# Kernel optimization log

Hardware: AMD Instinct MI355X
Metric: run time of the kernel (lower is better)

Reference implementation:

```python
import jax, jax.numpy as jnp
import numpy as np

C = 96          # channels (= output_dim)
NUM_HEADS = 6
DILS = (1, 2, 3)
KS_ATT = 3      # dilate-attention kernel size
KS_COR = 5      # self-correlation kernel size
PAD_COR = 2
LN_EPS = 1e-5


def _unfold(x, k, dil, pad):
    # torch.nn.Unfold(kernel=k, dilation=dil, padding=pad, stride=1)
    # x: [B, C, H, W] -> [B, C, k*k, H, W] (channel-major, kernel row-major)
    B, c, H, W = x.shape
    xp = jnp.pad(x, ((0, 0), (0, 0), (pad, pad), (pad, pad)))
    patches = [xp[:, :, i * dil:i * dil + H, j * dil:j * dil + W]
               for i in range(k) for j in range(k)]
    return jnp.stack(patches, axis=2)


def _layernorm(x, g, b):
    m = jnp.mean(x, axis=-1, keepdims=True)
    v = jnp.mean((x - m) ** 2, axis=-1, keepdims=True)
    return (x - m) * jax.lax.rsqrt(v + LN_EPS) * g + b


def _dilate_attn(q, k, v, dil, head_dim, scale):
    # q,k,v: [B, cb, H, W] with cb = C // num_dilation
    B, cb, H, W = q.shape
    heads = cb // head_dim
    qf = q.reshape(B, heads, head_dim, H * W)                                  # bhdn
    kp = _unfold(k, KS_ATT, dil, dil).reshape(B, heads, head_dim, KS_ATT * KS_ATT, H * W)
    attn = jax.nn.softmax(jnp.einsum('bhdn,bhdkn->bhnk', qf, kp) * scale, axis=-1)
    vp = _unfold(v, KS_ATT, dil, dil).reshape(B, heads, head_dim, KS_ATT * KS_ATT, H * W)
    out = jnp.einsum('bhnk,bhdkn->bnhd', attn, vp)                             # [B,HW,heads,hd]
    return out.reshape(B, H, W, cb)


def _forward(x, g1, b1, Wqkv, bqkv, Wproj, bproj, g2, b2, W1, bm1, W2, bm2):
    B, Cc, H, W = x.shape
    nd = len(DILS)
    head_dim = Cc // NUM_HEADS
    scale = head_dim ** (-0.5)

    xh = jnp.transpose(x, (0, 2, 3, 1))                                        # [B,H,W,C]

    # --- MultiDilatelocalAttention block ---
    y = _layernorm(xh, g1, b1)
    qkv = jnp.einsum('bhwc,oc->bhwo', y, Wqkv) + bqkv                          # 1x1 conv == linear
    qkv = jnp.transpose(qkv, (0, 3, 1, 2)).reshape(B, 3, nd, Cc // nd, H, W)
    outs = []
    for i, d in enumerate(DILS):
        outs.append(_dilate_attn(qkv[:, 0, i], qkv[:, 1, i], qkv[:, 2, i], d, head_dim, scale))
    a = jnp.concatenate(outs, axis=-1)                                         # dilation-major channels
    a = a @ Wproj.T + bproj
    xh = xh + a

    # --- MLP block ---
    z = _layernorm(xh, g2, b2)
    z = jax.nn.gelu(z @ W1.T + bm1, approximate=False) @ W2.T + bm2
    xh = xh + z

    # --- self-correlation ---
    xc = jnp.transpose(xh, (0, 3, 1, 2))                                       # [B,C,H,W]
    xc = jax.nn.relu(xc)
    nrm = jnp.sqrt(jnp.sum(xc * xc, axis=1, keepdims=True))
    xc = xc / jnp.maximum(nrm, 1e-12)                                          # F.normalize dim=1
    pat = _unfold(xc, KS_COR, 1, PAD_COR)                                      # [B,C,25,H,W]
    out = pat.reshape(B, Cc, KS_COR, KS_COR, H, W) * xc[:, :, None, None]
    return jnp.transpose(out, (0, 1, 4, 5, 2, 3))                              # [B,C,H,W,5,5]


def setup_inputs() -> dict:
    key = jax.random.key(0)
    ks = jax.random.split(key, 8)
    B, H, W = 8, 64, 64
    s = 0.02
    return {
        'x': jax.random.normal(ks[0], (B, C, H, W), jnp.float32),
        'g1': jnp.ones((C,), jnp.float32),
        'b1': jnp.zeros((C,), jnp.float32),
        'Wqkv': jax.random.normal(ks[1], (3 * C, C), jnp.float32) * s,
        'bqkv': jnp.zeros((3 * C,), jnp.float32),
        'Wproj': jax.random.normal(ks[2], (C, C), jnp.float32) * s,
        'bproj': jnp.zeros((C,), jnp.float32),
        'g2': jnp.ones((C,), jnp.float32),
        'b2': jnp.zeros((C,), jnp.float32),
        'W1': jax.random.normal(ks[3], (4 * C, C), jnp.float32) * s,
        'bm1': jnp.zeros((4 * C,), jnp.float32),
        'W2': jax.random.normal(ks[4], (C, 4 * C), jnp.float32) * s,
        'bm2': jnp.zeros((C,), jnp.float32),
    }


def reference(x, g1, b1, Wqkv, bqkv, Wproj, bproj, g2, b2, W1, bm1, W2, bm2):
    return _forward(x, g1, b1, Wqkv, bqkv, Wproj, bproj, g2, b2, W1, bm1, W2, bm2)
```

## Files before the change

### kernel.cpp

```cpp
#include <hip/hip_runtime.h>
#include <math.h>

#define NN 4096
#define BN 32768
#define CSTR 66

using short8 = __attribute__((ext_vector_type(8))) short;
using f32x4  = __attribute__((ext_vector_type(4))) float;
typedef unsigned short ushort_t;

__device__ inline unsigned f2bfu(float f) {
    unsigned u = __builtin_bit_cast(unsigned, f);
    u += 0x7FFFu + ((u >> 16) & 1u);
    return u >> 16;
}
__device__ inline ushort_t f2bf(float f) { return (ushort_t)f2bfu(f); }
__device__ inline unsigned pack2(float a, float b) { return f2bfu(a) | (f2bfu(b) << 16); }
__device__ inline float bflo(unsigned u) { return __builtin_bit_cast(float, u << 16); }
__device__ inline float bfhi(unsigned u) { return __builtin_bit_cast(float, u & 0xFFFF0000u); }

__device__ inline float gelu_f(float v) {
    float xx = v * 0.70710678118654752f;
    float a  = fabsf(xx);
    float t  = 1.0f / (1.0f + 0.3275911f * a);
    float p  = t*(0.254829592f + t*(-0.284496736f + t*(1.421413741f + t*(-1.453152027f + t*1.061405429f))));
    float erfv = 1.0f - p * __expf(-xx*xx);
    erfv = copysignf(erfv, xx);
    return 0.5f * v * (1.0f + erfv);
}

__device__ inline void stage_w(const unsigned* __restrict__ wbf, int stage,
                               ushort_t* dst, int wv, int lane) {
    const unsigned* src = wbf + (long)stage * 5120 + lane * 4;
    #pragma unroll
    for (int i = 0; i < 5; ++i) {
        int chunk = wv + 4 * i;
        __builtin_amdgcn_global_load_lds(
            (const __attribute__((address_space(1))) unsigned*)(src + chunk * 256),
            (__attribute__((address_space(3))) unsigned*)(dst + chunk * 512),
            16, 0, 0);
    }
}

#define MFMA_GEMM6(ACC, APTR, BPTR)                                              \
    _Pragma("unroll")                                                            \
    for (int kc = 0; kc < 3; ++kc) {                                             \
        short8 a_ = *(const short8*)&(APTR)[(wv*16 + ln)*104 + kc*32 + qd*8];    \
        _Pragma("unroll")                                                        \
        for (int t = 0; t < 6; ++t) {                                            \
            short8 b_ = *(const short8*)&(BPTR)[(t*16 + ln)*104 + kc*32 + qd*8]; \
            ACC[t] = __builtin_amdgcn_mfma_f32_16x16x32_bf16(a_, b_, ACC[t], 0, 0, 0); \
        }                                                                        \
    }

#define MFMA_GEMM6R(ACC, AF, BPTR)                                               \
    _Pragma("unroll")                                                            \
    for (int kc = 0; kc < 3; ++kc) {                                             \
        _Pragma("unroll")                                                        \
        for (int t = 0; t < 6; ++t) {                                            \
            short8 b_ = *(const short8*)&(BPTR)[(t*16 + ln)*104 + kc*32 + qd*8]; \
            ACC[t] = __builtin_amdgcn_mfma_f32_16x16x32_bf16(AF[kc], b_, ACC[t], 0, 0, 0); \
        }                                                                        \
    }

#define LN_FRAGS(AF, CS, G, B)                                                   \
    {                                                                            \
        const int p_ = wv*16 + ln;                                               \
        float xv_[24]; float s_ = 0.f, ss_ = 0.f;                                \
        _Pragma("unroll")                                                        \
        for (int kc = 0; kc < 3; ++kc)                                           \
            _Pragma("unroll")                                                    \
            for (int j = 0; j < 8; ++j) {                                        \
                float v_ = (CS)[(kc*32 + qd*8 + j)*CSTR + p_];                   \
                xv_[kc*8+j] = v_; s_ += v_; ss_ += v_*v_;                        \
            }                                                                    \
        s_  += __shfl_xor(s_, 16);  s_  += __shfl_xor(s_, 32);                   \
        ss_ += __shfl_xor(ss_, 16); ss_ += __shfl_xor(ss_, 32);                  \
        float m_ = s_ * (1.f/96.f);                                              \
        float rs_ = rsqrtf(ss_ * (1.f/96.f) - m_*m_ + 1e-5f);                    \
        _Pragma("unroll")                                                        \
        for (int kc = 0; kc < 3; ++kc)                                           \
            _Pragma("unroll")                                                    \
            for (int h = 0; h < 2; ++h) {                                        \
                int c0_ = kc*32 + qd*8 + h*4;                                    \
                float4 g4_ = *(const float4*)&(G)[c0_];                          \
                float4 b4_ = *(const float4*)&(B)[c0_];                          \
                (AF)[kc][h*4+0] = (short)f2bf((xv_[kc*8+h*4+0]-m_)*rs_*g4_.x + b4_.x); \
                (AF)[kc][h*4+1] = (short)f2bf((xv_[kc*8+h*4+1]-m_)*rs_*g4_.y + b4_.y); \
                (AF)[kc][h*4+2] = (short)f2bf((xv_[kc*8+h*4+2]-m_)*rs_*g4_.z + b4_.z); \
                (AF)[kc][h*4+3] = (short)f2bf((xv_[kc*8+h*4+3]-m_)*rs_*g4_.w + b4_.w); \
            }                                                                    \
    }

__global__ __launch_bounds__(256) void k0_pack(
    const float* __restrict__ Wqkv, const float* __restrict__ Wproj,
    const float* __restrict__ W1, const float* __restrict__ W2,
    unsigned* __restrict__ wbf)
{
    int d = blockIdx.x * 256 + threadIdx.x;
    int s = d / 5120, r = d - s * 5120;
    int o = r / 52, qp = r - o * 52;
    unsigned val = 0u;
    if (o < 96 && qp < 48) {
        int q = qp * 2;
        float2 w2;
        if (s == 0)      w2 = *(const float2*)&Wqkv[(long)o * 96 + q];
        else if (s == 1) w2 = *(const float2*)&Wqkv[(long)(96 + o) * 96 + q];
        else if (s == 2) w2 = *(const float2*)&Wqkv[(long)(192 + o) * 96 + q];
        else if (s == 3) w2 = *(const float2*)&Wproj[(long)o * 96 + q];
        else if (((s - 4) & 1) == 0) { int kb = (s - 4) >> 1; w2 = *(const float2*)&W1[(long)(kb * 96 + o) * 96 + q]; }
        else                         { int kb = (s - 4) >> 1; w2 = *(const float2*)&W2[(long)o * 384 + kb * 96 + q]; }
        val = pack2(w2.x, w2.y);
    }
    wbf[d] = val;
}

__global__ __launch_bounds__(256, 2) void k1_ln_kv(
    const float* __restrict__ x, const float* __restrict__ g1, const float* __restrict__ b1,
    const float* __restrict__ bqkv, const unsigned* __restrict__ wbf,
    unsigned* __restrict__ kvt32)
{
    __shared__ __align__(16) float    Cs[96 * CSTR];
    __shared__ __align__(16) ushort_t Bs[2][10240];
    const int tid = threadIdx.x;
    const int bid = blockIdx.x;
    const int wg  = ((bid & 7) << 6) | (bid >> 3);
    const long bn0 = (long)wg << 6;
    const int b  = (int)(bn0 >> 12);
    const int n0 = (int)(bn0 & 4095);
    const int lane = tid & 63, wv = tid >> 6;
    const int ln = lane & 15, qd = lane >> 4;

    stage_w(wbf, 1, &Bs[0][0], wv, lane);
    stage_w(wbf, 2, &Bs[1][0], wv, lane);
    for (int i = 0; i < 6; ++i) {
        int idx = i * 256 + tid;
        int c = idx >> 4, p4 = idx & 15;
        float4 v = *(const float4*)&x[((long)(b * 96 + c) << 12) + n0 + p4 * 4];
        float* dst = &Cs[c * CSTR + p4 * 4];
        dst[0] = v.x; dst[1] = v.y; dst[2] = v.z; dst[3] = v.w;
    }
    __syncthreads();
    short8 af[3];
    LN_FRAGS(af, Cs, g1, b1);
    f32x4 acck[6];
    #pragma unroll
    for (int t = 0; t < 6; ++t) acck[t] = (f32x4){0.f,0.f,0.f,0.f};
    MFMA_GEMM6R(acck, af, Bs[0]);
    __syncthreads();
    #pragma unroll
    for (int t = 0; t < 6; ++t)
        #pragma unroll
        for (int r = 0; r < 4; ++r)
            Cs[(t*16 + ln)*CSTR + (wv*16 + qd*4 + r)] = acck[t][r];
    __syncthreads();
    f32x4 accv[6];
    #pragma unroll
    for (int t = 0; t < 6; ++t) accv[t] = (f32x4){0.f,0.f,0.f,0.f};
    for (int i = 0; i < 12; ++i) {
        int idx = i * 256 + tid;
        int cp = idx / 64, p = idx % 64;
        int c = 2 * cp;
        kvt32[((long)(b*96 + cp) << 12) + n0 + p] =
            pack2(Cs[c*CSTR + p] + bqkv[96 + c], Cs[(c+1)*CSTR + p] + bqkv[96 + c + 1]);
    }
    MFMA_GEMM6R(accv, af, Bs[1]);
    __syncthreads();
    #pragma unroll
    for (int t = 0; t < 6; ++t)
        #pragma unroll
        for (int r = 0; r < 4; ++r)
            Cs[(t*16 + ln)*CSTR + (wv*16 + qd*4 + r)] = accv[t][r];
    __syncthreads();
    for (int i = 0; i < 12; ++i) {
        int idx = i * 256 + tid;
        int cp = idx / 64, p = idx % 64;
        int c = 2 * cp;
        kvt32[((long)(b*96 + 48 + cp) << 12) + n0 + p] =
            pack2(Cs[c*CSTR + p] + bqkv[192 + c], Cs[(c+1)*CSTR + p] + bqkv[192 + c + 1]);
    }
}

__global__ __launch_bounds__(256, 2) void k2345(
    const unsigned* __restrict__ kvt32, const float* __restrict__ x,
    const float* __restrict__ g1, const float* __restrict__ b1,
    const float* __restrict__ bqkv, const unsigned* __restrict__ wbf,
    const float* __restrict__ bproj,
    const float* __restrict__ g2, const float* __restrict__ b2,
    const float* __restrict__ bm1, const float* __restrict__ bm2,
    float* __restrict__ xcn)
{
    __shared__ __align__(16) float    Cs[96 * CSTR];
    __shared__ __align__(16) ushort_t As[64 * 104];
    __shared__ __align__(16) ushort_t Bs[2][10240];
    __shared__ float lnr[64];
    ushort_t* Hs = (ushort_t*)Cs;
    const int tid = threadIdx.x;
    const int bid = blockIdx.x;
    const int wg  = ((bid & 7) << 6) | (bid >> 3);
    const long bn0 = (long)wg << 6;
    const int b  = (int)(bn0 >> 12);
    const int n0 = (int)(bn0 & 4095);
    const int h0 = n0 >> 6;
    const int lane = tid & 63, wv = tid >> 6;
    const int ln = lane & 15, qd = lane >> 4;

    stage_w(wbf, 0, &Bs[0][0], wv, lane);
    stage_w(wbf, 3, &Bs[1][0], wv, lane);
    for (int i = 0; i < 6; ++i) {
        int idx = i * 256 + tid;
        int c = idx >> 4, p4 = idx & 15;
        float4 v = *(const float4*)&x[((long)(b * 96 + c) << 12) + n0 + p4 * 4];
        float* dst = &Cs[c * CSTR + p4 * 4];
        dst[0] = v.x; dst[1] = v.y; dst[2] = v.z; dst[3] = v.w;
    }
    __syncthreads();
    {
        short8 af[3];
        LN_FRAGS(af, Cs, g1, b1);
        f32x4 acc[6];
        #pragma unroll
        for (int t = 0; t < 6; ++t) acc[t] = (f32x4){0.f,0.f,0.f,0.f};
        MFMA_GEMM6R(acc, af, Bs[0]);
        #pragma unroll
        for (int t = 0; t < 6; ++t) {
            float bias = bqkv[t*16 + ln];
            #pragma unroll
            for (int r = 0; r < 4; ++r)
                As[(wv*16 + qd*4 + r)*104 + t*16 + ln] = f2bf(acc[t][r] + bias);
        }
    }
    __syncthreads();
    stage_w(wbf, 4, &Bs[0][0], wv, lane);
    for (int it = 0; it < 2; ++it) {
        int item = it * 256 + tid;
        if (item < 384) {
            int p = item & 63;
            int r = item >> 6;
            int head = r & 1, di = r >> 1;
            int dil = di + 1;
            int cp0 = di*16 + head*8;
            const unsigned* K = kvt32 + ((long)(b*96 +      cp0) << 12);
            const unsigned* V = kvt32 + ((long)(b*96 + 48 + cp0) << 12);
            int w = p;

            float q[16];
            #pragma unroll
            for (int j = 0; j < 8; ++j) {
                unsigned u = *(const unsigned*)&As[p * 104 + 2*(cp0 + j)];
                q[2*j] = bflo(u); q[2*j+1] = bfhi(u);
            }
            float logits[9];
            #pragma unroll
            for (int ki = 0; ki < 3; ++ki)
                #pragma unroll
                for (int kj = 0; kj < 3; ++kj) {
                    int hh = h0 + (ki-1)*dil, ww = w + (kj-1)*dil;
                    float l = 0.f;
                    if ((unsigned)hh < 64u && (unsigned)ww < 64u) {
                        int nn = (hh << 6) + ww;
                        #pragma unroll
                        for (int j = 0; j < 8; ++j) {
                            unsigned u = K[((long)j << 12) + nn];
                            l += q[2*j] * bflo(u) + q[2*j+1] * bfhi(u);
                        }
                    }
                    logits[ki*3 + kj] = l * 0.25f;
                }
            float m = logits[0];
            #pragma unroll
            for (int k = 1; k < 9; ++k) m = fmaxf(m, logits[k]);
            float e[9], s = 0.f;
            #pragma unroll
            for (int k = 0; k < 9; ++k) { e[k] = __expf(logits[k] - m); s += e[k]; }
            float inv = 1.f / s;
            float o[16];
            #pragma unroll
            for (int d = 0; d < 16; ++d) o[d] = 0.f;
            #pragma unroll
            for (int ki = 0; ki < 3; ++ki)
                #pragma unroll
                for (int kj = 0; kj < 3; ++kj) {
                    int hh = h0 + (ki-1)*dil, ww = w + (kj-1)*dil;
                    if ((unsigned)hh < 64u && (unsigned)ww < 64u) {
                        int nn = (hh << 6) + ww;
                        float wgt = e[ki*3 + kj] * inv;
                        #pragma unroll
                        for (int j = 0; j < 8; ++j) {
                            unsigned u = V[((long)j << 12) + nn];
                            o[2*j]   += wgt * bflo(u);
                            o[2*j+1] += wgt * bfhi(u);
                        }
                    }
                }
            #pragma unroll
            for (int j = 0; j < 8; ++j)
                *(unsigned*)&As[p * 104 + 2*(cp0 + j)] = pack2(o[2*j], o[2*j+1]);
        }
    }
    __syncthreads();
    float resid[24];
    {
        f32x4 acc[6];
        #pragma unroll
        for (int t = 0; t < 6; ++t) acc[t] = (f32x4){0.f,0.f,0.f,0.f};
        MFMA_GEMM6(acc, As, Bs[1]);
        #pragma unroll
        for (int t = 0; t < 6; ++t) {
            int oc = t*16 + ln;
            float bias = bproj[oc];
            #pragma unroll
            for (int r = 0; r < 4; ++r) {
                int p = wv*16 + qd*4 + r;
                float v = acc[t][r] + bias + Cs[oc*CSTR + p];
                resid[t*4 + r] = v;
                Cs[oc*CSTR + p] = v;
            }
        }
    }
    __syncthreads();
    stage_w(wbf, 5, &Bs[1][0], wv, lane);
    short8 zf[3];
    LN_FRAGS(zf, Cs, g2, b2);
    __syncthreads();
    f32x4 acc2[6];
    #pragma unroll
    for (int t = 0; t < 6; ++t) acc2[t] = (f32x4){0.f,0.f,0.f,0.f};
    for (int kb = 0; kb < 4; ++kb) {
        f32x4 acch[6];
        #pragma unroll
        for (int t = 0; t < 6; ++t) acch[t] = (f32x4){0.f,0.f,0.f,0.f};
        MFMA_GEMM6R(acch, zf, Bs[0]);
        #pragma unroll
        for (int t = 0; t < 6; ++t) {
            float bias = bm1[kb*96 + t*16 + ln];
            #pragma unroll
            for (int r = 0; r < 4; ++r)
                Hs[(wv*16 + qd*4 + r)*104 + t*16 + ln] = f2bf(gelu_f(acch[t][r] + bias));
        }
        __syncthreads();
        if (kb < 3) stage_w(wbf, 6 + 2*kb, &Bs[0][0], wv, lane);
        MFMA_GEMM6(acc2, Hs, Bs[1]);
        __syncthreads();
        if (kb < 3) stage_w(wbf, 7 + 2*kb, &Bs[1][0], wv, lane);
    }
    #pragma unroll
    for (int t = 0; t < 6; ++t) {
        int oc = t*16 + ln;
        float bias = bm2[oc];
        #pragma unroll
        for (int r = 0; r < 4; ++r) {
            int p = wv*16 + qd*4 + r;
            float v = acc2[t][r] + bias + resid[t*4 + r];
            Cs[oc*CSTR + p] = fmaxf(v, 0.f);
        }
    }
    __syncthreads();
    {
        int p = tid >> 2, part = tid & 3, c0 = part * 24;
        float ss = 0.f;
        for (int c = c0; c < c0 + 24; ++c) { float v = Cs[c*CSTR + p]; ss += v*v; }
        ss += __shfl_xor(ss, 1); ss += __shfl_xor(ss, 2);
        if (part == 0) lnr[p] = 1.f / fmaxf(sqrtf(ss), 1e-12f);
    }
    __syncthreads();
    for (int i = 0; i < 12; ++i) {
        int idx = i * 256 + tid;
        int p = idx / 48, cp = idx % 48;
        float inv = lnr[p];
        float2 v = make_float2(Cs[(2*cp)*CSTR + p] * inv, Cs[(2*cp+1)*CSTR + p] * inv);
        *(float2*)&xcn[(bn0 + p) * 96 + 2*cp] = v;
    }
}

__global__ __launch_bounds__(256) void k6_selfcorr(
    const float* __restrict__ xcn, float* __restrict__ out)
{
    __shared__ float xt[5 * 20 * 97];
    const int tid = threadIdx.x;
    const int wc = blockIdx.x;
    const int h  = blockIdx.y;
    const int b  = blockIdx.z;
    const int w0 = wc * 16;

    const f32x4* xcn4 = (const f32x4*)xcn;
    for (int i = 0; i < 10; ++i) {
        int idx = i * 256 + tid;
        if (idx < 2400) {
            int r = idx / 480;
            int rem = idx - r * 480;
            int wi = rem / 24, c4 = rem - wi * 24;
            int hh = h + r - 2, ww = w0 + wi - 2;
            f32x4 v = (f32x4){0.f, 0.f, 0.f, 0.f};
            if ((unsigned)hh < 64u && (unsigned)ww < 64u)
                v = xcn4[(((long)b << 12) + (hh << 6) + ww) * 24 + c4];
            float* dst = &xt[(r * 20 + wi) * 97 + c4 * 4];
            dst[0] = v[0]; dst[1] = v[1]; dst[2] = v[2]; dst[3] = v[3];
        }
    }
    __syncthreads();
    f32x4* out4 = (f32x4*)out;
    const long ob4 = (long)b * 2457600 + (long)h * 400 + wc * 100;
    for (int i = 0; i < 38; ++i) {
        int idx = i * 256 + tid;
        if (idx < 9600) {
            int c = idx / 100;
            int r4 = idx - c * 100;
            f32x4 v;
            #pragma unroll
            for (int j = 0; j < 4; ++j) {
                int r = r4 * 4 + j;
                int lw = r / 25, k = r - lw * 25;
                int ki = k / 5, kj = k - ki * 5;
                float center = xt[(42 + lw) * 97 + c];
                float neigh  = xt[(ki * 20 + lw + kj) * 97 + c];
                v[j] = center * neigh;
            }
            __builtin_nontemporal_store(v, &out4[ob4 + (long)c * 25600 + r4]);
        }
    }
}

extern "C" void kernel_launch(void* const* d_in, const int* in_sizes, int n_in,
                              void* d_out, int out_size, void* d_ws, size_t ws_size,
                              hipStream_t stream)
{
    const float* x     = (const float*)d_in[0];
    const float* g1    = (const float*)d_in[1];
    const float* b1    = (const float*)d_in[2];
    const float* Wqkv  = (const float*)d_in[3];
    const float* bqkv  = (const float*)d_in[4];
    const float* Wproj = (const float*)d_in[5];
    const float* bproj = (const float*)d_in[6];
    const float* g2    = (const float*)d_in[7];
    const float* b2    = (const float*)d_in[8];
    const float* W1    = (const float*)d_in[9];
    const float* bm1   = (const float*)d_in[10];
    const float* W2    = (const float*)d_in[11];
    const float* bm2   = (const float*)d_in[12];
    float* out = (float*)d_out;

    char* w = (char*)d_ws;
    unsigned* wbf   = (unsigned*)w;  w += 12 * 20480;
    unsigned* kvt32 = (unsigned*)w;  w += (size_t)BN * 192 * 2;
    float*    xcn   = (float*)w;

    k0_pack    <<<240, 256, 0, stream>>>(Wqkv, Wproj, W1, W2, wbf);
    k1_ln_kv   <<<BN / 64, 256, 0, stream>>>(x, g1, b1, bqkv, wbf, kvt32);
    k2345      <<<BN / 64, 256, 0, stream>>>(kvt32, x, g1, b1, bqkv, wbf,
                                             bproj, g2, b2, bm1, bm2, xcn);
    k6_selfcorr<<<dim3(4, 64, 8), 256, 0, stream>>>(xcn, out);
}
```

Baseline: 396.0 us.

## Fuse K/V projection kernel into attention kernel with inter-block flag synchronization

Merges the separate LN+K/V projection kernel into the main attention/MLP kernel, so LayerNorm and the x tile load happen once per block. Each block computes Q, K and V, writes K/V to global memory, publishes a per-row release flag, and spin-waits on flags from the 7 neighbouring rows it needs for the dilated neighbourhood. The residual x is kept in registers instead of being re-read from shared memory. This removes one kernel launch and the duplicated LN work, but relies on neighbouring blocks being co-resident or already finished. With 512 blocks at 2 per CU that should hold, though a deadlock is possible if scheduling order or occupancy differs.

```diff
diff --git a/kernel.cpp b/kernel.cpp
--- a/kernel.cpp
+++ b/kernel.cpp
@@ -115,76 +115,11 @@
     wbf[d] = val;
 }
 
-__global__ __launch_bounds__(256, 2) void k1_ln_kv(
-    const float* __restrict__ x, const float* __restrict__ g1, const float* __restrict__ b1,
-    const float* __restrict__ bqkv, const unsigned* __restrict__ wbf,
-    unsigned* __restrict__ kvt32)
-{
-    __shared__ __align__(16) float    Cs[96 * CSTR];
-    __shared__ __align__(16) ushort_t Bs[2][10240];
-    const int tid = threadIdx.x;
-    const int bid = blockIdx.x;
-    const int wg  = ((bid & 7) << 6) | (bid >> 3);
-    const long bn0 = (long)wg << 6;
-    const int b  = (int)(bn0 >> 12);
-    const int n0 = (int)(bn0 & 4095);
-    const int lane = tid & 63, wv = tid >> 6;
-    const int ln = lane & 15, qd = lane >> 4;
-
-    stage_w(wbf, 1, &Bs[0][0], wv, lane);
-    stage_w(wbf, 2, &Bs[1][0], wv, lane);
-    for (int i = 0; i < 6; ++i) {
-        int idx = i * 256 + tid;
-        int c = idx >> 4, p4 = idx & 15;
-        float4 v = *(const float4*)&x[((long)(b * 96 + c) << 12) + n0 + p4 * 4];
-        float* dst = &Cs[c * CSTR + p4 * 4];
-        dst[0] = v.x; dst[1] = v.y; dst[2] = v.z; dst[3] = v.w;
-    }
-    __syncthreads();
-    short8 af[3];
-    LN_FRAGS(af, Cs, g1, b1);
-    f32x4 acck[6];
-    #pragma unroll
-    for (int t = 0; t < 6; ++t) acck[t] = (f32x4){0.f,0.f,0.f,0.f};
-    MFMA_GEMM6R(acck, af, Bs[0]);
-    __syncthreads();
-    #pragma unroll
-    for (int t = 0; t < 6; ++t)
-        #pragma unroll
-        for (int r = 0; r < 4; ++r)
-            Cs[(t*16 + ln)*CSTR + (wv*16 + qd*4 + r)] = acck[t][r];
-    __syncthreads();
-    f32x4 accv[6];
-    #pragma unroll
-    for (int t = 0; t < 6; ++t) accv[t] = (f32x4){0.f,0.f,0.f,0.f};
-    for (int i = 0; i < 12; ++i) {
-        int idx = i * 256 + tid;
-        int cp = idx / 64, p = idx % 64;
-        int c = 2 * cp;
-        kvt32[((long)(b*96 + cp) << 12) + n0 + p] =
-            pack2(Cs[c*CSTR + p] + bqkv[96 + c], Cs[(c+1)*CSTR + p] + bqkv[96 + c + 1]);
-    }
-    MFMA_GEMM6R(accv, af, Bs[1]);
-    __syncthreads();
-    #pragma unroll
-    for (int t = 0; t < 6; ++t)
-        #pragma unroll
-        for (int r = 0; r < 4; ++r)
-            Cs[(t*16 + ln)*CSTR + (wv*16 + qd*4 + r)] = accv[t][r];
-    __syncthreads();
-    for (int i = 0; i < 12; ++i) {
-        int idx = i * 256 + tid;
-        int cp = idx / 64, p = idx % 64;
-        int c = 2 * cp;
-        kvt32[((long)(b*96 + 48 + cp) << 12) + n0 + p] =
-            pack2(Cs[c*CSTR + p] + bqkv[192 + c], Cs[(c+1)*CSTR + p] + bqkv[192 + c + 1]);
-    }
-}
-
-__global__ __launch_bounds__(256, 2) void k2345(
-    const unsigned* __restrict__ kvt32, const float* __restrict__ x,
+__global__ __launch_bounds__(256, 2) void kfused(
+    const float* __restrict__ x,
     const float* __restrict__ g1, const float* __restrict__ b1,
     const float* __restrict__ bqkv, const unsigned* __restrict__ wbf,
+    unsigned* __restrict__ kvt32, unsigned* __restrict__ flags,
     const float* __restrict__ bproj,
     const float* __restrict__ g2, const float* __restrict__ b2,
     const float* __restrict__ bm1, const float* __restrict__ bm2,
@@ -206,7 +141,7 @@
     const int ln = lane & 15, qd = lane >> 4;
 
     stage_w(wbf, 0, &Bs[0][0], wv, lane);
-    stage_w(wbf, 3, &Bs[1][0], wv, lane);
+    stage_w(wbf, 1, &Bs[1][0], wv, lane);
     for (int i = 0; i < 6; ++i) {
         int idx = i * 256 + tid;
         int c = idx >> 4, p4 = idx & 15;
@@ -215,23 +150,77 @@
         dst[0] = v.x; dst[1] = v.y; dst[2] = v.z; dst[3] = v.w;
     }
     __syncthreads();
-    {
-        short8 af[3];
-        LN_FRAGS(af, Cs, g1, b1);
-        f32x4 acc[6];
-        #pragma unroll
-        for (int t = 0; t < 6; ++t) acc[t] = (f32x4){0.f,0.f,0.f,0.f};
-        MFMA_GEMM6R(acc, af, Bs[0]);
-        #pragma unroll
-        for (int t = 0; t < 6; ++t) {
-            float bias = bqkv[t*16 + ln];
-            #pragma unroll
-            for (int r = 0; r < 4; ++r)
-                As[(wv*16 + qd*4 + r)*104 + t*16 + ln] = f2bf(acc[t][r] + bias);
-        }
-    }
+    short8 af[3];
+    LN_FRAGS(af, Cs, g1, b1);
+    float xres[24];
+    #pragma unroll
+    for (int t = 0; t < 6; ++t)
+        #pragma unroll
+        for (int r = 0; r < 4; ++r)
+            xres[t*4 + r] = Cs[(t*16 + ln)*CSTR + (wv*16 + qd*4 + r)];
+    f32x4 accq[6], acck[6];
+    #pragma unroll
+    for (int t = 0; t < 6; ++t) { accq[t] = (f32x4){0.f,0.f,0.f,0.f}; acck[t] = (f32x4){0.f,0.f,0.f,0.f}; }
+    MFMA_GEMM6R(accq, af, Bs[0]);
+    MFMA_GEMM6R(acck, af, Bs[1]);
+    #pragma unroll
+    for (int t = 0; t < 6; ++t) {
+        float bias = bqkv[t*16 + ln];
+        #pragma unroll
+        for (int r = 0; r < 4; ++r)
+            As[(wv*16 + qd*4 + r)*104 + t*16 + ln] = f2bf(accq[t][r] + bias);
+    }
+    __syncthreads();
+    stage_w(wbf, 2, &Bs[0][0], wv, lane);
+    stage_w(wbf, 3, &Bs[1][0], wv, lane);
+    #pragma unroll
+    for (int t = 0; t < 6; ++t)
+        #pragma unroll
+        for (int r = 0; r < 4; ++r)
+            Cs[(t*16 + ln)*CSTR + (wv*16 + qd*4 + r)] = acck[t][r];
+    __syncthreads();
+    f32x4 accv[6];
+    #pragma unroll
+    for (int t = 0; t < 6; ++t) accv[t] = (f32x4){0.f,0.f,0.f,0.f};
+    for (int i = 0; i < 12; ++i) {
+        int idx = i * 256 + tid;
+        int cp = idx / 64, p = idx % 64;
+        int c = 2 * cp;
+        kvt32[((long)(b*96 + cp) << 12) + n0 + p] =
+            pack2(Cs[c*CSTR + p] + bqkv[96 + c], Cs[(c+1)*CSTR + p] + bqkv[96 + c + 1]);
+    }
+    MFMA_GEMM6R(accv, af, Bs[0]);
     __syncthreads();
     stage_w(wbf, 4, &Bs[0][0], wv, lane);
+    #pragma unroll
+    for (int t = 0; t < 6; ++t)
+        #pragma unroll
+        for (int r = 0; r < 4; ++r)
+            Cs[(t*16 + ln)*CSTR + (wv*16 + qd*4 + r)] = accv[t][r];
+    __syncthreads();
+    for (int i = 0; i < 12; ++i) {
+        int idx = i * 256 + tid;
+        int cp = idx / 64, p = idx % 64;
+        int c = 2 * cp;
+        kvt32[((long)(b*96 + 48 + cp) << 12) + n0 + p] =
+            pack2(Cs[c*CSTR + p] + bqkv[192 + c], Cs[(c+1)*CSTR + p] + bqkv[192 + c + 1]);
+    }
+
+    __threadfence();
+    __syncthreads();
+    if (tid == 0)
+        __hip_atomic_store(&flags[wg], 1u, __ATOMIC_RELEASE, __HIP_MEMORY_SCOPE_AGENT);
+    if (tid < 7) {
+        int hh = h0 + (int)tid - 3;
+        if ((unsigned)hh < 64u) {
+            const unsigned* f = &flags[b * 64 + hh];
+            while (__hip_atomic_load(f, __ATOMIC_ACQUIRE, __HIP_MEMORY_SCOPE_AGENT) == 0u)
+                __builtin_amdgcn_s_sleep(1);
+        }
+    }
+    __syncthreads();
+    __threadfence();
+
     for (int it = 0; it < 2; ++it) {
         int item = it * 256 + tid;
         if (item < 384) {
@@ -312,7 +301,7 @@
             #pragma unroll
             for (int r = 0; r < 4; ++r) {
                 int p = wv*16 + qd*4 + r;
-                float v = acc[t][r] + bias + Cs[oc*CSTR + p];
+                float v = acc[t][r] + bias + xres[t*4 + r];
                 resid[t*4 + r] = v;
                 Cs[oc*CSTR + p] = v;
             }
@@ -443,11 +432,12 @@
     char* w = (char*)d_ws;
     unsigned* wbf   = (unsigned*)w;  w += 12 * 20480;
     unsigned* kvt32 = (unsigned*)w;  w += (size_t)BN * 192 * 2;
+    unsigned* flags = (unsigned*)w;  w += 4096;
     float*    xcn   = (float*)w;
 
-    k0_pack    <<<240, 256, 0, stream>>>(Wqkv, Wproj, W1, W2, wbf);
-    k1_ln_kv   <<<BN / 64, 256, 0, stream>>>(x, g1, b1, bqkv, wbf, kvt32);
-    k2345      <<<BN / 64, 256, 0, stream>>>(kvt32, x, g1, b1, bqkv, wbf,
-                                             bproj, g2, b2, bm1, bm2, xcn);
+    hipMemsetAsync(flags, 0, 512 * sizeof(unsigned), stream);
+    k0_pack<<<240, 256, 0, stream>>>(Wqkv, Wproj, W1, W2, wbf);
+    kfused <<<BN / 64, 256, 0, stream>>>(x, g1, b1, bqkv, wbf, kvt32, flags,
+                                         bproj, g2, b2, bm1, bm2, xcn);
     k6_selfcorr<<<dim3(4, 64, 8), 256, 0, stream>>>(xcn, out);
 }
```

Result: slower. 486.9 us (+23.0%).
